# Kernel optimization log

Hardware: AMD Instinct MI355X
Metric: run time of the kernel (lower is better)

Reference implementation:

```python
import jax, jax.numpy as jnp
import numpy as np

WINDOW_SIZE = 11
SIGMA = 1.5
C1 = 0.01 ** 2
C2 = 0.03 ** 2


def _gaussian_window(window_size, sigma, channel):
    x = np.arange(window_size, dtype=np.float64)
    g = np.exp(-((x - window_size // 2) ** 2) / (2.0 * sigma ** 2))
    g = g / g.sum()
    w2d = np.outer(g, g).astype(np.float32)  # [K,K]
    # depthwise kernel: [C, 1, K, K] (OIHW with feature_group_count=C)
    return jnp.asarray(np.broadcast_to(w2d, (channel, 1, window_size, window_size)).copy())


def _depthwise_blur(x, window):
    pad = WINDOW_SIZE // 2
    return jax.lax.conv_general_dilated(
        x, window,
        window_strides=(1, 1),
        padding=[(pad, pad), (pad, pad)],
        feature_group_count=x.shape[1],
        dimension_numbers=('NCHW', 'OIHW', 'NCHW'))


def setup_inputs() -> dict:
    key = jax.random.key(0)
    k1, k2 = jax.random.split(key)
    shape = (16, 3, 512, 512)
    image = jax.random.uniform(k1, shape, dtype=jnp.float32)
    target = jax.random.uniform(k2, shape, dtype=jnp.float32)
    return {"image": image, "target": target}


def reference(image, target):
    channel = image.shape[1]
    window = _gaussian_window(WINDOW_SIZE, SIGMA, channel)

    mu1 = _depthwise_blur(image, window)
    mu2 = _depthwise_blur(target, window)
    mu1_sq = mu1 * mu1
    mu2_sq = mu2 * mu2
    mu1_mu2 = mu1 * mu2

    sigma1_sq = _depthwise_blur(image * image, window) - mu1_sq
    sigma2_sq = _depthwise_blur(target * target, window) - mu2_sq
    sigma12 = _depthwise_blur(image * target, window) - mu1_mu2

    ssim_map = ((2.0 * mu1_mu2 + C1) * (2.0 * sigma12 + C2)) / (
        (mu1_sq + mu2_sq + C1) * (sigma1_sq + sigma2_sq + C2))
    return 1.0 - jnp.mean(ssim_map)
```

## Files before the change

### kernel.cpp

```cpp
#include <hip/hip_runtime.h>
#include <hip/hip_fp16.h>
#include <math.h>


#define HH 512
#define WW 512
#define NPLANES 48
#define G_TILES 8
#define NBLOCKS 768

typedef _Float16 f16x8 __attribute__((ext_vector_type(8)));
typedef _Float16 f16x4 __attribute__((ext_vector_type(4)));
typedef float f32x4 __attribute__((ext_vector_type(4)));

#define RAW_STRIDE 208
#define RAW_PLANE  9984
#define OUTH_CSTR  104
#define LDS_TOTAL  39936

struct WParam { float A, B; };

__global__ void ssim_init_out(float* out) { out[0] = 1.0f; }

__device__ __forceinline__ void barrier_nodrain() {
    asm volatile("s_waitcnt lgkmcnt(0)" ::: "memory");
    __builtin_amdgcn_s_barrier();
    __builtin_amdgcn_sched_barrier(0);
}

__global__ __launch_bounds__(256, 4)
void ssim_mfma(const float* __restrict__ img, const float* __restrict__ tgt,
               float* __restrict__ out, WParam wp) {
    __shared__ alignas(16) char lds[LDS_TOTAL];
    __shared__ float wsum[4];

    const int tid  = threadIdx.x;
    const int wid  = tid >> 6;
    const int lane = tid & 63;
    const int cl   = lane & 15;
    const int am   = lane >> 4;

    const int it0 = tid,       ir0 = it0 / 10, ig0 = it0 - 10 * ir0;
    const int it1 = tid + 256, ir1 = it1 / 10, ig1 = it1 - 10 * ir1;
    const bool has1 = (tid < 164);

    float4 Xa[2], Xb[2], Ya[2], Yb[2];

    auto load_tile = [&](int tlin) {
        const int p   = tlin >> 7;
        const int rem = tlin & 127;
        const int R0  = (rem >> 3) * 32;
        const int C0  = (rem & 7) * 64;
        const float* ip = img + (size_t)p * (HH * WW);
        const float* tp = tgt + (size_t)p * (HH * WW);
        #pragma unroll
        for (int s = 0; s < 2; ++s) {
            if (s == 1 && !has1) break;
            int r   = s ? ir1 : ir0;
            int grp = s ? ig1 : ig0;
            int gr  = R0 - 5 + r;
            int gc0 = C0 - 8 + grp * 8;
            float4 xa = make_float4(0.f,0.f,0.f,0.f), xb = xa, ya = xa, yb = xa;
            if ((unsigned)gr < (unsigned)HH) {
                const float* xr = ip + (size_t)gr * WW;
                const float* yr = tp + (size_t)gr * WW;
                if ((unsigned)gc0 <= (unsigned)(WW - 4)) {
                    xa = *(const float4*)(xr + gc0);
                    ya = *(const float4*)(yr + gc0);
                }
                if ((unsigned)(gc0 + 4) <= (unsigned)(WW - 4)) {
                    xb = *(const float4*)(xr + gc0 + 4);
                    yb = *(const float4*)(yr + gc0 + 4);
                }
            }
            Xa[s] = xa; Xb[s] = xb; Ya[s] = ya; Yb[s] = yb;
        }
    };

    auto write_tile = [&]() {
        #pragma unroll
        for (int s = 0; s < 2; ++s) {
            if (s == 1 && !has1) break;
            int r   = s ? ir1 : ir0;
            int grp = s ? ig1 : ig0;
            float fx[8] = {Xa[s].x,Xa[s].y,Xa[s].z,Xa[s].w,
                           Xb[s].x,Xb[s].y,Xb[s].z,Xb[s].w};
            float fy[8] = {Ya[s].x,Ya[s].y,Ya[s].z,Ya[s].w,
                           Yb[s].x,Yb[s].y,Yb[s].z,Yb[s].w};
            f16x8 hx, hy;
            #pragma unroll
            for (int j = 0; j < 8; ++j) {
                hx[j] = (_Float16)fx[j];
                hy[j] = (_Float16)fy[j];
            }
            f16x8 hs = hx*hx + hy*hy;
            f16x8 hp = hx*hy;
            char* base = lds + r * RAW_STRIDE + grp * 16;
            *(f16x8*)(base + 0*RAW_PLANE) = hx;
            *(f16x8*)(base + 1*RAW_PLANE) = hy;
            *(f16x8*)(base + 2*RAW_PLANE) = hs;
            *(f16x8*)(base + 3*RAW_PLANE) = hp;
        }
    };

    const int base_t = blockIdx.x * G_TILES;
    load_tile(base_t);

    for (int i = tid; i < LDS_TOTAL / 4; i += 256)
        ((float*)lds)[i] = 0.f;

    f16x8 Bh, Av;
    #pragma unroll
    for (int j = 0; j < 8; ++j) {
        int k = 8 * am + j;
        int ih = k - cl - 3;
        float th = (float)(ih - 5);
        Bh[j] = ((unsigned)ih <= 10u) ? (_Float16)(wp.A * exp2f(-wp.B * th * th))
                                      : (_Float16)0.f;
        int iv = k - cl;
        float tv = (float)(iv - 5);
        Av[j] = ((unsigned)iv <= 10u) ? (_Float16)(wp.A * exp2f(-wp.B * tv * tv))
                                      : (_Float16)0.f;
    }
    __syncthreads();

    const float C1 = 1e-4f, C2 = 9e-4f;
    float lsum = 0.f;

    for (int g = 0; g < G_TILES; ++g) {
        write_tile();
        if (g + 1 < G_TILES) load_tile(base_t + g + 1);
        barrier_nodrain();

        {
            char* plane = lds + wid * RAW_PLANE;
            const int abase = cl * RAW_STRIDE + am * 16;
            f16x8 Af[3][4];
            #pragma unroll
            for (int mt = 0; mt < 3; ++mt)
                #pragma unroll
                for (int nt = 0; nt < 4; ++nt)
                    Af[mt][nt] = *(const f16x8*)(plane + abase
                                                 + mt * 16 * RAW_STRIDE + nt * 32);
            __builtin_amdgcn_sched_barrier(0);
            const int wbase = cl * OUTH_CSTR + am * 8;
            #pragma unroll
            for (int nt = 0; nt < 4; ++nt) {
                #pragma unroll
                for (int mt = 0; mt < 3; ++mt) {
                    f32x4 acc = {0.f, 0.f, 0.f, 0.f};
                    acc = __builtin_amdgcn_mfma_f32_16x16x32_f16(
                              Af[mt][nt], Bh, acc, 0, 0, 0);
                    f16x4 h;
                    #pragma unroll
                    for (int j = 0; j < 4; ++j) h[j] = (_Float16)acc[j];
                    *(f16x4*)(plane + wbase + nt * 16 * OUTH_CSTR + mt * 32) = h;
                }
            }
        }
        barrier_nodrain();

        {
            const int bbase = (16 * wid + cl) * OUTH_CSTR + am * 16;
            f32x4 accv[4][2];
            #pragma unroll
            for (int q = 0; q < 4; ++q) {
                #pragma unroll
                for (int mt = 0; mt < 2; ++mt) {
                    f16x8 Bf = *(const f16x8*)(lds + q * RAW_PLANE + bbase + mt * 32);
                    f32x4 acc = {0.f, 0.f, 0.f, 0.f};
                    accv[q][mt] = __builtin_amdgcn_mfma_f32_16x16x32_f16(
                                      Av, Bf, acc, 0, 0, 0);
                }
            }
            #pragma unroll
            for (int mt = 0; mt < 2; ++mt) {
                #pragma unroll
                for (int j = 0; j < 4; ++j) {
                    float mu1 = accv[0][mt][j], mu2 = accv[1][mt][j];
                    float bss = accv[2][mt][j], bxy = accv[3][mt][j];
                    float mu1s = mu1*mu1, mu2s = mu2*mu2, mu12 = mu1*mu2;
                    float ssum = bss - mu1s - mu2s;
                    float s12  = bxy - mu12;
                    float num = (2.f*mu12 + C1) * (2.f*s12 + C2);
                    float den = (mu1s + mu2s + C1) * (ssum + C2);
                    lsum = fmaf(num, __builtin_amdgcn_rcpf(den), lsum);
                }
            }
        }
        barrier_nodrain();
    }

    for (int off = 32; off > 0; off >>= 1)
        lsum += __shfl_down(lsum, off, 64);
    if (lane == 0) wsum[wid] = lsum;
    __syncthreads();
    if (tid == 0) {
        float bsum = wsum[0] + wsum[1] + wsum[2] + wsum[3];
        const float invN = 1.0f / (float)((size_t)NPLANES * HH * WW);
        atomicAdd(out, -bsum * invN);
    }
}

extern "C" void kernel_launch(void* const* d_in, const int* in_sizes, int n_in,
                              void* d_out, int out_size, void* d_ws, size_t ws_size,
                              hipStream_t stream) {
    const float* img = (const float*)d_in[0];
    const float* tgt = (const float*)d_in[1];
    float* out = (float*)d_out;

    double s = 0.0;
    for (int i = 0; i < 11; ++i) {
        double d = (double)(i - 5);
        s += exp(-(d * d) / 4.5);
    }
    WParam wp;
    wp.A = (float)(1.0 / s);
    wp.B = (float)(M_LOG2E / 4.5);

    ssim_init_out<<<1, 1, 0, stream>>>(out);
    ssim_mfma<<<NBLOCKS, 256, 0, stream>>>(img, tgt, out, wp);
}
```

Baseline: 40.73 us.

## Fuse horizontal and vertical MFMA blur passes in registers, store only x/y in LDS

Squares and cross products are now computed from the loaded x/y fragments in registers instead of being staged as two extra LDS planes. The horizontal blur result is fed straight from MFMA accumulators into the vertical blur as 16x16x16 operands, which removes the intermediate LDS write/read and one barrier per tile. LDS per block is halved, allowing more resident blocks, and the grid is reshaped to 1024 blocks of 6 tiles. The trade-off is extra MFMAs and redundant f16 product computation per wave.

```diff
diff --git a/kernel.cpp b/kernel.cpp
--- a/kernel.cpp
+++ b/kernel.cpp
@@ -5,9 +5,10 @@
 
 #define HH 512
 #define WW 512
+#define HW (HH*WW)
 #define NPLANES 48
-#define G_TILES 8
-#define NBLOCKS 768
+#define G_TILES 6
+#define NBLOCKS 1024
 
 typedef _Float16 f16x8 __attribute__((ext_vector_type(8)));
 typedef _Float16 f16x4 __attribute__((ext_vector_type(4)));
@@ -15,8 +16,7 @@
 
 #define RAW_STRIDE 208
 #define RAW_PLANE  9984
-#define OUTH_CSTR  104
-#define LDS_TOTAL  39936
+#define LDS_TOTAL  19968
 
 struct WParam { float A, B; };
 
@@ -51,8 +51,8 @@
         const int rem = tlin & 127;
         const int R0  = (rem >> 3) * 32;
         const int C0  = (rem & 7) * 64;
-        const float* ip = img + (size_t)p * (HH * WW);
-        const float* tp = tgt + (size_t)p * (HH * WW);
+        const float* ip = img + (size_t)p * HW;
+        const float* tp = tgt + (size_t)p * HW;
         #pragma unroll
         for (int s = 0; s < 2; ++s) {
             if (s == 1 && !has1) break;
@@ -83,23 +83,18 @@
             if (s == 1 && !has1) break;
             int r   = s ? ir1 : ir0;
             int grp = s ? ig1 : ig0;
-            float fx[8] = {Xa[s].x,Xa[s].y,Xa[s].z,Xa[s].w,
-                           Xb[s].x,Xb[s].y,Xb[s].z,Xb[s].w};
-            float fy[8] = {Ya[s].x,Ya[s].y,Ya[s].z,Ya[s].w,
-                           Yb[s].x,Yb[s].y,Yb[s].z,Yb[s].w};
             f16x8 hx, hy;
-            #pragma unroll
-            for (int j = 0; j < 8; ++j) {
-                hx[j] = (_Float16)fx[j];
-                hy[j] = (_Float16)fy[j];
-            }
-            f16x8 hs = hx*hx + hy*hy;
-            f16x8 hp = hx*hy;
+            hx[0]=(_Float16)Xa[s].x; hx[1]=(_Float16)Xa[s].y;
+            hx[2]=(_Float16)Xa[s].z; hx[3]=(_Float16)Xa[s].w;
+            hx[4]=(_Float16)Xb[s].x; hx[5]=(_Float16)Xb[s].y;
+            hx[6]=(_Float16)Xb[s].z; hx[7]=(_Float16)Xb[s].w;
+            hy[0]=(_Float16)Ya[s].x; hy[1]=(_Float16)Ya[s].y;
+            hy[2]=(_Float16)Ya[s].z; hy[3]=(_Float16)Ya[s].w;
+            hy[4]=(_Float16)Yb[s].x; hy[5]=(_Float16)Yb[s].y;
+            hy[6]=(_Float16)Yb[s].z; hy[7]=(_Float16)Yb[s].w;
             char* base = lds + r * RAW_STRIDE + grp * 16;
             *(f16x8*)(base + 0*RAW_PLANE) = hx;
             *(f16x8*)(base + 1*RAW_PLANE) = hy;
-            *(f16x8*)(base + 2*RAW_PLANE) = hs;
-            *(f16x8*)(base + 3*RAW_PLANE) = hp;
         }
     };
 
@@ -109,18 +104,26 @@
     for (int i = tid; i < LDS_TOTAL / 4; i += 256)
         ((float*)lds)[i] = 0.f;
 
-    f16x8 Bh, Av;
+    f16x8 Bh;
     #pragma unroll
     for (int j = 0; j < 8; ++j) {
-        int k = 8 * am + j;
-        int ih = k - cl - 3;
-        float th = (float)(ih - 5);
-        Bh[j] = ((unsigned)ih <= 10u) ? (_Float16)(wp.A * exp2f(-wp.B * th * th))
+        int ih = 8*am + j - cl - 3;
+        float t = (float)(ih - 5);
+        Bh[j] = ((unsigned)ih <= 10u) ? (_Float16)(wp.A * exp2f(-wp.B*t*t))
                                       : (_Float16)0.f;
-        int iv = k - cl;
-        float tv = (float)(iv - 5);
-        Av[j] = ((unsigned)iv <= 10u) ? (_Float16)(wp.A * exp2f(-wp.B * tv * tv))
-                                      : (_Float16)0.f;
+    }
+    f16x4 Av1, Av2;
+    #pragma unroll
+    for (int j = 0; j < 4; ++j) {
+        int k = 4*am + j;
+        int i1 = k - cl;
+        float t1 = (float)(i1 - 5);
+        Av1[j] = ((unsigned)i1 <= 10u) ? (_Float16)(wp.A * exp2f(-wp.B*t1*t1))
+                                       : (_Float16)0.f;
+        int i2 = k + 16 - cl;
+        float t2 = (float)(i2 - 5);
+        Av2[j] = ((unsigned)i2 <= 10u) ? (_Float16)(wp.A * exp2f(-wp.B*t2*t2))
+                                       : (_Float16)0.f;
     }
     __syncthreads();
 
@@ -133,52 +136,47 @@
         barrier_nodrain();
 
         {
-            char* plane = lds + wid * RAW_PLANE;
-            const int abase = cl * RAW_STRIDE + am * 16;
-            f16x8 Af[3][4];
+            const int abase = cl * RAW_STRIDE + 32 * wid + am * 16;
+            f16x8 hx3[3], hy3[3];
             #pragma unroll
-            for (int mt = 0; mt < 3; ++mt)
-                #pragma unroll
-                for (int nt = 0; nt < 4; ++nt)
-                    Af[mt][nt] = *(const f16x8*)(plane + abase
-                                                 + mt * 16 * RAW_STRIDE + nt * 32);
-            __builtin_amdgcn_sched_barrier(0);
-            const int wbase = cl * OUTH_CSTR + am * 8;
-            #pragma unroll
-            for (int nt = 0; nt < 4; ++nt) {
-                #pragma unroll
-                for (int mt = 0; mt < 3; ++mt) {
-                    f32x4 acc = {0.f, 0.f, 0.f, 0.f};
-                    acc = __builtin_amdgcn_mfma_f32_16x16x32_f16(
-                              Af[mt][nt], Bh, acc, 0, 0, 0);
-                    f16x4 h;
-                    #pragma unroll
-                    for (int j = 0; j < 4; ++j) h[j] = (_Float16)acc[j];
-                    *(f16x4*)(plane + wbase + nt * 16 * OUTH_CSTR + mt * 32) = h;
-                }
-            }
-        }
-        barrier_nodrain();
-
-        {
-            const int bbase = (16 * wid + cl) * OUTH_CSTR + am * 16;
+            for (int mt = 0; mt < 3; ++mt) {
+                hx3[mt] = *(const f16x8*)(lds + (16*mt) * RAW_STRIDE + abase);
+                hy3[mt] = *(const f16x8*)(lds + RAW_PLANE + (16*mt) * RAW_STRIDE + abase);
+            }
+
             f32x4 accv[4][2];
             #pragma unroll
             for (int q = 0; q < 4; ++q) {
+                f32x4 Dh[3];
                 #pragma unroll
-                for (int mt = 0; mt < 2; ++mt) {
-                    f16x8 Bf = *(const f16x8*)(lds + q * RAW_PLANE + bbase + mt * 32);
-                    f32x4 acc = {0.f, 0.f, 0.f, 0.f};
-                    accv[q][mt] = __builtin_amdgcn_mfma_f32_16x16x32_f16(
-                                      Av, Bf, acc, 0, 0, 0);
-                }
-            }
+                for (int mt = 0; mt < 3; ++mt) {
+                    f16x8 A = (q == 0) ? hx3[mt]
+                            : (q == 1) ? hy3[mt]
+                            : (q == 2) ? (f16x8)(hx3[mt]*hx3[mt] + hy3[mt]*hy3[mt])
+                                       : (f16x8)(hx3[mt]*hy3[mt]);
+                    f32x4 zz = {0.f, 0.f, 0.f, 0.f};
+                    Dh[mt] = __builtin_amdgcn_mfma_f32_16x16x32_f16(A, Bh, zz, 0, 0, 0);
+                }
+                #pragma unroll
+                for (int mtv = 0; mtv < 2; ++mtv) {
+                    f16x4 B1, B2;
+                    #pragma unroll
+                    for (int j = 0; j < 4; ++j) {
+                        B1[j] = (_Float16)Dh[mtv][j];
+                        B2[j] = (_Float16)Dh[mtv+1][j];
+                    }
+                    f32x4 zz = {0.f, 0.f, 0.f, 0.f};
+                    f32x4 acc = __builtin_amdgcn_mfma_f32_16x16x16f16(Av2, B2, zz, 0, 0, 0);
+                    accv[q][mtv] = __builtin_amdgcn_mfma_f32_16x16x16f16(Av1, B1, acc, 0, 0, 0);
+                }
+            }
+
             #pragma unroll
-            for (int mt = 0; mt < 2; ++mt) {
+            for (int mtv = 0; mtv < 2; ++mtv) {
                 #pragma unroll
                 for (int j = 0; j < 4; ++j) {
-                    float mu1 = accv[0][mt][j], mu2 = accv[1][mt][j];
-                    float bss = accv[2][mt][j], bxy = accv[3][mt][j];
+                    float mu1 = accv[0][mtv][j], mu2 = accv[1][mtv][j];
+                    float bss = accv[2][mtv][j], bxy = accv[3][mtv][j];
                     float mu1s = mu1*mu1, mu2s = mu2*mu2, mu12 = mu1*mu2;
                     float ssum = bss - mu1s - mu2s;
                     float s12  = bxy - mu12;
```

Measured after the change: 40.28 us. Within noise of the previous version (-1.1%).
